# Optimization experiments

Measured on AMD Instinct MI355X. Metric: run time of the kernel, lower is better.

The kernel has to match this reference:

```python
import jax, jax.numpy as jnp
import numpy as np

NH = 16   # n_heads
HD = 64   # head_size
EMB = 1024  # n_embd = NH * HD
B, T = 4, 2048


def setup_inputs() -> dict:
    key = jax.random.key(0)
    k1, k2, k3 = jax.random.split(key, 3)
    x = jax.random.normal(k1, (B, T, EMB), dtype=jnp.float32)
    # torch Linear(in, out, bias=False): weight [out,in]; we store transposed [in,out]
    W_attn = jax.random.normal(k2, (EMB, 3 * NH * HD), dtype=jnp.float32) * (EMB ** -0.5)
    W_proj = jax.random.normal(k3, (NH * HD, EMB), dtype=jnp.float32) * ((NH * HD) ** -0.5)
    b_proj = jnp.zeros((EMB,), dtype=jnp.float32)
    return {"x": x, "W_attn": W_attn, "W_proj": W_proj, "b_proj": b_proj}


def reference(x, W_attn, W_proj, b_proj):
    Bq, Tq, C = x.shape
    qkv = x @ W_attn                      # [B,T,3*Nh*H]
    qs, ks, vs = jnp.split(qkv, 3, axis=2)
    def to_heads(t):                      # [B,T,Nh*H] -> [B,Nh,T,H]
        return t.reshape(Bq, Tq, NH, HD).transpose(0, 2, 1, 3)
    q, k, v = to_heads(qs), to_heads(ks), to_heads(vs)
    scores = jnp.einsum('bnth,bnsh->bnts', q, k) * (HD ** -0.5)  # [B,Nh,T,T]
    causal = jnp.tril(jnp.ones((Tq, Tq), dtype=bool))
    scores = jnp.where(causal, scores, -jnp.inf)
    attn = jax.nn.softmax(scores, axis=-1)
    # dropout is identity in eval mode
    y = jnp.einsum('bnts,bnsh->bnth', attn, v)                   # [B,Nh,T,H]
    y = y.transpose(0, 2, 1, 3).reshape(Bq, Tq, NH * HD)
    return y @ W_proj + b_proj
```

## Files before the change

kernel.cpp:

```cpp
#include <hip/hip_runtime.h>
#include <hip/hip_bf16.h>

#define NH 16
#define HD 64
#define EMB 1024
#define BB 4
#define TT 2048
#define MTOT (BB*TT)
#define N1 (3*NH*HD)
#define KD EMB

#define BM 128
#define BN 128
#define BK 32

#define QSCALE 0.18033688011112042f
#define FMAX 14.0f

typedef __bf16 bf16x8 __attribute__((ext_vector_type(8)));
typedef __bf16 bf16x4 __attribute__((ext_vector_type(4)));
typedef float  f32x4  __attribute__((ext_vector_type(4)));
typedef __hip_bfloat16 hbf;

__device__ __forceinline__ void async_copy16(const hbf* g, hbf* l) {
    __builtin_amdgcn_global_load_lds(
        (const __attribute__((address_space(1))) void*)g,
        (__attribute__((address_space(3))) void*)l, 16, 0, 0);
}

__device__ __forceinline__ bf16x4 pack4(float x0, float x1, float x2, float x3) {
    union { bf16x4 v; hbf a[4]; } u;
    u.a[0] = __float2bfloat16(x0);
    u.a[1] = __float2bfloat16(x1);
    u.a[2] = __float2bfloat16(x2);
    u.a[3] = __float2bfloat16(x3);
    return u.v;
}


__global__ __launch_bounds__(256) void f32_to_bf16_v4(const float* __restrict__ in,
                                                      hbf* __restrict__ out, int n4) {
    int i = blockIdx.x * blockDim.x + threadIdx.x;
    if (i < n4) {
        float4 v = ((const float4*)in)[i];
        *(bf16x4*)(out + 4 * (size_t)i) = pack4(v.x, v.y, v.z, v.w);
    }
}

__global__ __launch_bounds__(256) void f32_to_bf16_T(const float* __restrict__ in,
                                                     hbf* __restrict__ out, int R, int C) {
    __shared__ float T[64][65];
    int bc = blockIdx.x % (C / 64), br = blockIdx.x / (C / 64);
    int r0 = br * 64, c0 = bc * 64;
    int tr = threadIdx.x >> 6, tc = threadIdx.x & 63;
    #pragma unroll
    for (int i = 0; i < 16; ++i)
        T[4 * i + tr][tc] = in[(size_t)(r0 + 4 * i + tr) * C + c0 + tc];
    __syncthreads();
    #pragma unroll
    for (int i = 0; i < 16; ++i)
        out[(size_t)(c0 + 4 * i + tr) * R + r0 + tc] = __float2bfloat16(T[tc][4 * i + tr]);
}


#define GEMM_STAGE(Sdst, Gsrc, ld)                                            \
    {                                                                         \
        _Pragma("unroll")                                                     \
        for (int q = 0; q < 2; ++q) {                                         \
            int e = q * 2048 + tid * 8;                                       \
            int row = e >> 5, col = e & 31;                                   \
            async_copy16(Gsrc + (size_t)row * (ld) + col,                     \
                         Sdst + q * 2048 + (tid & ~63) * 8);                  \
        }                                                                     \
    }

__global__ __launch_bounds__(256) void gemm_qkv(
    const hbf* __restrict__ A, const hbf* __restrict__ Bt,
    hbf* __restrict__ qh, hbf* __restrict__ kh, hbf* __restrict__ vt)
{
    __shared__ __align__(16) hbf As[BM * BK];
    __shared__ __align__(16) hbf Bs[BN * BK];
    int tid = threadIdx.x;
    int wv = tid >> 6, lane = tid & 63;
    int g = lane >> 4, c = lane & 15;
    int wr = wv >> 1, wc = wv & 1;
    int bn = blockIdx.x % (N1 / BN);
    int bm = blockIdx.x / (N1 / BN);
    int m0 = bm * BM, n0 = bn * BN;

    f32x4 acc[4][4];
    #pragma unroll
    for (int i = 0; i < 4; ++i)
        #pragma unroll
        for (int j = 0; j < 4; ++j) acc[i][j] = (f32x4){0.f, 0.f, 0.f, 0.f};

    for (int k0 = 0; k0 < KD; k0 += BK) {
        const hbf* Ag = A  + (size_t)m0 * KD + k0;
        const hbf* Bg = Bt + (size_t)n0 * KD + k0;
        GEMM_STAGE(As, Ag, KD);
        GEMM_STAGE(Bs, Bg, KD);
        __syncthreads();
        bf16x8 af[4], bf[4];
        #pragma unroll
        for (int mi = 0; mi < 4; ++mi)
            af[mi] = *(const bf16x8*)(As + (wr * 64 + mi * 16 + c) * BK + g * 8);
        #pragma unroll
        for (int ni = 0; ni < 4; ++ni)
            bf[ni] = *(const bf16x8*)(Bs + (wc * 64 + ni * 16 + c) * BK + g * 8);
        #pragma unroll
        for (int mi = 0; mi < 4; ++mi)
            #pragma unroll
            for (int ni = 0; ni < 4; ++ni)
                acc[mi][ni] = __builtin_amdgcn_mfma_f32_16x16x32_bf16(af[mi], bf[ni], acc[mi][ni], 0, 0, 0);
        __syncthreads();
    }

    int colbase = n0 + wc * 64;
    int which = colbase / (NH * HD);
    int h = (colbase % (NH * HD)) / HD;
    int b = m0 / TT;
    float scale = (which == 0) ? QSCALE : 1.0f;
    if (which < 2) {
        hbf* dst = (which == 0) ? qh : kh;
        dst += ((size_t)b * NH + h) * TT * HD;
        #pragma unroll
        for (int mi = 0; mi < 4; ++mi)
            #pragma unroll
            for (int ni = 0; ni < 4; ++ni) {
                int d = ni * 16 + c;
                #pragma unroll
                for (int r = 0; r < 4; ++r) {
                    int t = (m0 + wr * 64 + mi * 16 + g * 4 + r) % TT;
                    dst[(size_t)t * HD + d] = __float2bfloat16(acc[mi][ni][r] * scale);
                }
            }
    } else {
        hbf* dst = vt + ((size_t)b * NH + h) * TT * HD;
        #pragma unroll
        for (int mi = 0; mi < 4; ++mi)
            #pragma unroll
            for (int ni = 0; ni < 4; ++ni) {
                int d = ni * 16 + c;
                #pragma unroll
                for (int r = 0; r < 4; ++r) {
                    int t = (m0 + wr * 64 + mi * 16 + g * 4 + r) % TT;
                    dst[(size_t)d * TT + t] = __float2bfloat16(acc[mi][ni][r]);
                }
            }
    }
}


__global__ __launch_bounds__(512, 4) void attn(
    const hbf* __restrict__ qh, const hbf* __restrict__ kh, const hbf* __restrict__ vt,
    hbf* __restrict__ y)
{
    __shared__ __align__(16) hbf Ks[128 * 64];
    __shared__ __align__(16) hbf Vs[64 * 128];
    __shared__ __align__(16) hbf Ps[8][16 * 64];

    int tid = threadIdx.x;
    int wv = tid >> 6, lane = tid & 63;
    int g = lane >> 4, c = lane & 15;
    int c7 = c & 7;

    int bh = blockIdx.x >> 3;
    int pi = blockIdx.x & 7;
    int b = bh >> 4, h = bh & 15;

    const hbf* Q = qh + (size_t)bh * TT * HD;
    const hbf* K = kh + (size_t)bh * TT * HD;
    const hbf* V = vt + (size_t)bh * TT * HD;
    hbf* Pq = &Ps[wv][0];

    union { bf16x8 v; hbf a[8]; } uo;
    #pragma unroll
    for (int i = 0; i < 8; ++i) uo.a[i] = __float2bfloat16(1.0f);
    const bf16x8 ones8 = uo.v;

    #pragma unroll
    for (int pass = 0; pass < 2; ++pass) {
        int sst = pass ? (15 - pi) : pi;
        int qb = sst * 128;
        int q0 = qb + wv * 16;
        int kend = q0 + 16;
        int kmax = qb + 128;

        bf16x8 aq0 = *(const bf16x8*)(Q + (size_t)(q0 + c) * HD + g * 8);
        bf16x8 aq1 = *(const bf16x8*)(Q + (size_t)(q0 + c) * HD + 32 + g * 8);

        f32x4 lacc = (f32x4){0.f, 0.f, 0.f, 0.f};
        f32x4 o[4];
        #pragma unroll
        for (int d = 0; d < 4; ++d) o[d] = (f32x4){0.f, 0.f, 0.f, 0.f};

        for (int k0 = 0; k0 < kmax; k0 += 128) {
            __syncthreads();
            #pragma unroll
            for (int it = 0; it < 2; ++it) {
                int e = it * 4096 + tid * 8;
                int key = e >> 6, sblk = (e >> 3) & 7;
                int dblk = sblk ^ (key & 7);
                async_copy16(K + (size_t)(k0 + key) * HD + dblk * 8,
                             Ks + it * 4096 + (tid & ~63) * 8);
            }
            #pragma unroll
            for (int it = 0; it < 2; ++it) {
                int e = it * 4096 + tid * 8;
                int dim = e >> 7, kb = (e >> 3) & 15;
                int skb = kb ^ (dim & 7);
                async_copy16(V + (size_t)dim * TT + k0 + skb * 8,
                             Vs + it * 4096 + (tid & ~63) * 8);
            }
            __syncthreads();

            #pragma unroll
            for (int ch = 0; ch < 2; ++ch) {
                int c64 = k0 + ch * 64;
                if (c64 < kend) {
                    f32x4 s[4];
                    #pragma unroll
                    for (int t = 0; t < 4; ++t) {
                        int kt = c64 + 16 * t;
                        if (kt < kend) {
                            int rb = (ch * 64 + 16 * t + c) * 64;
                            bf16x8 kf0 = *(const bf16x8*)(Ks + rb + ((g ^ c7) << 3));
                            bf16x8 kf1 = *(const bf16x8*)(Ks + rb + (((4 + g) ^ c7) << 3));
                            f32x4 a = (f32x4){-FMAX, -FMAX, -FMAX, -FMAX};
                            a = __builtin_amdgcn_mfma_f32_16x16x32_bf16(kf0, aq0, a, 0, 0, 0);
                            a = __builtin_amdgcn_mfma_f32_16x16x32_bf16(kf1, aq1, a, 0, 0, 0);
                            if (kt == q0) {
                                #pragma unroll
                                for (int r = 0; r < 4; ++r)
                                    a[r] = (g * 4 + r <= c) ? a[r] : -1e30f;
                            }
                            s[t] = a;
                        } else
                            s[t] = (f32x4){-1e30f, -1e30f, -1e30f, -1e30f};
                    }
                    #pragma unroll
                    for (int t = 0; t < 4; ++t) {
                        f32x4 e;
                        #pragma unroll
                        for (int r = 0; r < 4; ++r) e[r] = __builtin_amdgcn_exp2f(s[t][r]);
                        *(bf16x4*)(Pq + c * 64 + (((2 * t + (g >> 1)) ^ c7) << 3) + ((g & 1) << 2)) =
                            pack4(e[0], e[1], e[2], e[3]);
                    }
                    #pragma unroll
                    for (int sc = 0; sc < 2; ++sc) {
                        if (c64 + 32 * sc < kend) {
                            bf16x8 pf = *(const bf16x8*)(Pq + c * 64 + (((4 * sc + g) ^ c7) << 3));
                            lacc = __builtin_amdgcn_mfma_f32_16x16x32_bf16(ones8, pf, lacc, 0, 0, 0);
                            #pragma unroll
                            for (int d = 0; d < 4; ++d) {
                                int dim = d * 16 + c;
                                bf16x8 vf = *(const bf16x8*)(Vs + dim * 128 +
                                              (((ch * 8 + 4 * sc + g) ^ c7) << 3));
                                o[d] = __builtin_amdgcn_mfma_f32_16x16x32_bf16(vf, pf, o[d], 0, 0, 0);
                            }
                        }
                    }
                }
            }
        }

        float inv = 1.0f / lacc[0];
        #pragma unroll
        for (int d = 0; d < 4; ++d) {
            *(bf16x4*)(y + (size_t)(b * TT + q0 + c) * EMB + h * HD + d * 16 + g * 4) =
                pack4(o[d][0] * inv, o[d][1] * inv, o[d][2] * inv, o[d][3] * inv);
        }
    }
}


__global__ __launch_bounds__(256) void gemm_out(
    const hbf* __restrict__ A, const hbf* __restrict__ Bt,
    const float* __restrict__ bias, float* __restrict__ out)
{
    __shared__ __align__(16) hbf As[BM * BK];
    __shared__ __align__(16) hbf Bs[BN * BK];
    int tid = threadIdx.x;
    int wv = tid >> 6, lane = tid & 63;
    int g = lane >> 4, c = lane & 15;
    int wr = wv >> 1, wc = wv & 1;
    int bn = blockIdx.x % (EMB / BN);
    int bm = blockIdx.x / (EMB / BN);
    int m0 = bm * BM, n0 = bn * BN;

    f32x4 acc[4][4];
    #pragma unroll
    for (int i = 0; i < 4; ++i)
        #pragma unroll
        for (int j = 0; j < 4; ++j) acc[i][j] = (f32x4){0.f, 0.f, 0.f, 0.f};

    for (int k0 = 0; k0 < EMB; k0 += BK) {
        const hbf* Ag = A  + (size_t)m0 * EMB + k0;
        const hbf* Bg = Bt + (size_t)n0 * EMB + k0;
        GEMM_STAGE(As, Ag, EMB);
        GEMM_STAGE(Bs, Bg, EMB);
        __syncthreads();
        bf16x8 af[4], bf[4];
        #pragma unroll
        for (int mi = 0; mi < 4; ++mi)
            af[mi] = *(const bf16x8*)(As + (wr * 64 + mi * 16 + c) * BK + g * 8);
        #pragma unroll
        for (int ni = 0; ni < 4; ++ni)
            bf[ni] = *(const bf16x8*)(Bs + (wc * 64 + ni * 16 + c) * BK + g * 8);
        #pragma unroll
        for (int mi = 0; mi < 4; ++mi)
            #pragma unroll
            for (int ni = 0; ni < 4; ++ni)
                acc[mi][ni] = __builtin_amdgcn_mfma_f32_16x16x32_bf16(af[mi], bf[ni], acc[mi][ni], 0, 0, 0);
        __syncthreads();
    }

    #pragma unroll
    for (int mi = 0; mi < 4; ++mi)
        #pragma unroll
        for (int ni = 0; ni < 4; ++ni) {
            int col = n0 + wc * 64 + ni * 16 + c;
            float bv = bias[col];
            #pragma unroll
            for (int r = 0; r < 4; ++r) {
                int row = m0 + wr * 64 + mi * 16 + g * 4 + r;
                out[(size_t)row * EMB + col] = acc[mi][ni][r] + bv;
            }
        }
}


extern "C" void kernel_launch(void* const* d_in, const int* in_sizes, int n_in,
                              void* d_out, int out_size, void* d_ws, size_t ws_size,
                              hipStream_t stream)
{
    const float* x      = (const float*)d_in[0];
    const float* W_attn = (const float*)d_in[1];
    const float* W_proj = (const float*)d_in[2];
    const float* b_proj = (const float*)d_in[3];
    float* out = (float*)d_out;

    char* ws = (char*)d_ws;
    hbf* xb    = (hbf*)ws; ws += (size_t)MTOT * KD * 2;
    hbf* wab_t = (hbf*)ws; ws += (size_t)N1 * KD * 2;
    hbf* wpb_t = (hbf*)ws; ws += (size_t)EMB * EMB * 2;
    hbf* qh    = (hbf*)ws; ws += (size_t)MTOT * EMB * 2;
    hbf* kh    = (hbf*)ws; ws += (size_t)MTOT * EMB * 2;
    hbf* vt    = (hbf*)ws; ws += (size_t)MTOT * EMB * 2;
    hbf* yb    = (hbf*)ws; ws += (size_t)MTOT * EMB * 2;

    f32_to_bf16_v4<<<(MTOT * KD / 4 + 255) / 256, 256, 0, stream>>>(x, xb, MTOT * KD / 4);
    f32_to_bf16_T<<<(KD / 64) * (N1 / 64), 256, 0, stream>>>(W_attn, wab_t, KD, N1);
    f32_to_bf16_T<<<(KD / 64) * (EMB / 64), 256, 0, stream>>>(W_proj, wpb_t, KD, EMB);

    gemm_qkv<<<(MTOT / BM) * (N1 / BN), 256, 0, stream>>>(xb, wab_t, qh, kh, vt);
    attn<<<BB * NH * 8, 512, 0, stream>>>(qh, kh, vt, yb);
    gemm_out<<<(MTOT / BM) * (EMB / BN), 256, 0, stream>>>(yb, wpb_t, b_proj, out);
}
```

Measured before the change: 254.8 us.

## Replace both GEMMs with 8-wave double-buffered swizzled BK=64 kernel

```diff
diff --git a/kernel.cpp b/kernel.cpp
--- a/kernel.cpp
+++ b/kernel.cpp
@@ -10,10 +10,6 @@
 #define N1 (3*NH*HD)
 #define KD EMB
 
-#define BM 128
-#define BN 128
-#define BK 32
-
 #define QSCALE 0.18033688011112042f
 #define FMAX 14.0f
 
@@ -63,88 +59,143 @@
 }
 
 
-#define GEMM_STAGE(Sdst, Gsrc, ld)                                            \
-    {                                                                         \
-        _Pragma("unroll")                                                     \
-        for (int q = 0; q < 2; ++q) {                                         \
-            int e = q * 2048 + tid * 8;                                       \
-            int row = e >> 5, col = e & 31;                                   \
-            async_copy16(Gsrc + (size_t)row * (ld) + col,                     \
-                         Sdst + q * 2048 + (tid & ~63) * 8);                  \
-        }                                                                     \
-    }
-
-__global__ __launch_bounds__(256) void gemm_qkv(
+template<int NBN, int MODE>
+__global__ __launch_bounds__(512, 4) void gemm8(
     const hbf* __restrict__ A, const hbf* __restrict__ Bt,
-    hbf* __restrict__ qh, hbf* __restrict__ kh, hbf* __restrict__ vt)
+    hbf* __restrict__ qh, hbf* __restrict__ kh, hbf* __restrict__ vt,
+    const float* __restrict__ bias, float* __restrict__ out)
 {
-    __shared__ __align__(16) hbf As[BM * BK];
-    __shared__ __align__(16) hbf Bs[BN * BK];
+    constexpr int NKT = KD / 64;
+    __shared__ __align__(16) hbf As[2 * 128 * 64];
+    __shared__ __align__(16) hbf Bs[2 * 128 * 64];
+
     int tid = threadIdx.x;
     int wv = tid >> 6, lane = tid & 63;
     int g = lane >> 4, c = lane & 15;
-    int wr = wv >> 1, wc = wv & 1;
-    int bn = blockIdx.x % (N1 / BN);
-    int bm = blockIdx.x / (N1 / BN);
-    int m0 = bm * BM, n0 = bn * BN;
-
-    f32x4 acc[4][4];
+    int wm = wv >> 2, wn = wv & 3;
+    int bn = blockIdx.x % NBN, bm = blockIdx.x / NBN;
+    int m0 = bm * 128, n0 = bn * 128;
+
+    int sr0 = tid >> 3;
+    int sgc = (tid & 7) ^ (sr0 & 7);
+    const hbf* Asrc0 = A  + (size_t)(m0 + sr0) * KD + sgc * 8;
+    const hbf* Asrc1 = A  + (size_t)(m0 + 64 + sr0) * KD + sgc * 8;
+    const hbf* Bsrc0 = Bt + (size_t)(n0 + sr0) * KD + sgc * 8;
+    const hbf* Bsrc1 = Bt + (size_t)(n0 + 64 + sr0) * KD + sgc * 8;
+    int ldst0 = (tid & ~63) * 8;
+    int ldst1 = 4096 + (tid & ~63) * 8;
+
+#define STAGE_A8(tt, buf) { async_copy16(Asrc0 + (tt) * 64, As + (buf) * 8192 + ldst0); \
+                            async_copy16(Asrc1 + (tt) * 64, As + (buf) * 8192 + ldst1); }
+#define STAGE_B8(tt, buf) { async_copy16(Bsrc0 + (tt) * 64, Bs + (buf) * 8192 + ldst0); \
+                            async_copy16(Bsrc1 + (tt) * 64, Bs + (buf) * 8192 + ldst1); }
+
+    int xr = c & 7;
+    int aoff0 = (wm * 64 + c) * 64 + ((g ^ xr) << 3);
+    int aoff1 = (wm * 64 + c) * 64 + (((4 + g) ^ xr) << 3);
+    int boff0 = (wn * 32 + c) * 64 + ((g ^ xr) << 3);
+    int boff1 = (wn * 32 + c) * 64 + (((4 + g) ^ xr) << 3);
+
+    f32x4 acc[4][2];
     #pragma unroll
     for (int i = 0; i < 4; ++i)
         #pragma unroll
-        for (int j = 0; j < 4; ++j) acc[i][j] = (f32x4){0.f, 0.f, 0.f, 0.f};
-
-    for (int k0 = 0; k0 < KD; k0 += BK) {
-        const hbf* Ag = A  + (size_t)m0 * KD + k0;
-        const hbf* Bg = Bt + (size_t)n0 * KD + k0;
-        GEMM_STAGE(As, Ag, KD);
-        GEMM_STAGE(Bs, Bg, KD);
-        __syncthreads();
-        bf16x8 af[4], bf[4];
-        #pragma unroll
-        for (int mi = 0; mi < 4; ++mi)
-            af[mi] = *(const bf16x8*)(As + (wr * 64 + mi * 16 + c) * BK + g * 8);
-        #pragma unroll
-        for (int ni = 0; ni < 4; ++ni)
-            bf[ni] = *(const bf16x8*)(Bs + (wc * 64 + ni * 16 + c) * BK + g * 8);
-        #pragma unroll
-        for (int mi = 0; mi < 4; ++mi)
-            #pragma unroll
-            for (int ni = 0; ni < 4; ++ni)
-                acc[mi][ni] = __builtin_amdgcn_mfma_f32_16x16x32_bf16(af[mi], bf[ni], acc[mi][ni], 0, 0, 0);
-        __syncthreads();
+        for (int j = 0; j < 2; ++j) acc[i][j] = (f32x4){0.f, 0.f, 0.f, 0.f};
+
+    STAGE_A8(0, 0);
+    STAGE_B8(0, 0);
+    STAGE_A8(1, 1);
+    asm volatile("s_waitcnt vmcnt(2)" ::: "memory");
+    asm volatile("s_barrier" ::: "memory");
+    __builtin_amdgcn_sched_barrier(0);
+
+    for (int t = 0; t < NKT; ++t) {
+        int cur = t & 1;
+        const hbf* Ab = As + cur * 8192;
+        const hbf* Bb = Bs + cur * 8192;
+        bf16x8 af[4][2], bfr[2];
+        #pragma unroll
+        for (int i = 0; i < 4; ++i) {
+            af[i][0] = *(const bf16x8*)(Ab + aoff0 + i * 1024);
+            af[i][1] = *(const bf16x8*)(Ab + aoff1 + i * 1024);
+        }
+        bfr[0] = *(const bf16x8*)(Bb + boff0);
+        bfr[1] = *(const bf16x8*)(Bb + boff1);
+        if (t + 1 < NKT) STAGE_B8(t + 1, cur ^ 1);
+        __builtin_amdgcn_s_setprio(1);
+        #pragma unroll
+        for (int i = 0; i < 4; ++i) {
+            acc[i][0] = __builtin_amdgcn_mfma_f32_16x16x32_bf16(af[i][0], bfr[0], acc[i][0], 0, 0, 0);
+            acc[i][0] = __builtin_amdgcn_mfma_f32_16x16x32_bf16(af[i][1], bfr[1], acc[i][0], 0, 0, 0);
+        }
+        __builtin_amdgcn_s_setprio(0);
+        asm volatile("s_barrier" ::: "memory");
+        __builtin_amdgcn_sched_barrier(0);
+        bfr[0] = *(const bf16x8*)(Bb + boff0 + 1024);
+        bfr[1] = *(const bf16x8*)(Bb + boff1 + 1024);
+        if (t + 2 < NKT) STAGE_A8(t + 2, cur);
+        __builtin_amdgcn_s_setprio(1);
+        #pragma unroll
+        for (int i = 0; i < 4; ++i) {
+            acc[i][1] = __builtin_amdgcn_mfma_f32_16x16x32_bf16(af[i][0], bfr[0], acc[i][1], 0, 0, 0);
+            acc[i][1] = __builtin_amdgcn_mfma_f32_16x16x32_bf16(af[i][1], bfr[1], acc[i][1], 0, 0, 0);
+        }
+        __builtin_amdgcn_s_setprio(0);
+        if (t + 2 < NKT) { asm volatile("s_waitcnt vmcnt(2)" ::: "memory"); }
+        else             { asm volatile("s_waitcnt vmcnt(0)" ::: "memory"); }
+        asm volatile("s_barrier" ::: "memory");
+        __builtin_amdgcn_sched_barrier(0);
     }
 
-    int colbase = n0 + wc * 64;
-    int which = colbase / (NH * HD);
-    int h = (colbase % (NH * HD)) / HD;
-    int b = m0 / TT;
-    float scale = (which == 0) ? QSCALE : 1.0f;
-    if (which < 2) {
-        hbf* dst = (which == 0) ? qh : kh;
-        dst += ((size_t)b * NH + h) * TT * HD;
-        #pragma unroll
-        for (int mi = 0; mi < 4; ++mi)
-            #pragma unroll
-            for (int ni = 0; ni < 4; ++ni) {
-                int d = ni * 16 + c;
+#undef STAGE_A8
+#undef STAGE_B8
+
+    if constexpr (MODE == 0) {
+        int colbase = n0 + wn * 32;
+        int which = colbase >> 10;
+        int h = (colbase & 1023) >> 6;
+        int dbase = colbase & 63;
+        int b = m0 / TT;
+        int trow = (m0 % TT) + wm * 64;
+        if (which < 2) {
+            float scale = (which == 0) ? QSCALE : 1.0f;
+            hbf* dst = ((which == 0) ? qh : kh) + ((size_t)b * NH + h) * TT * HD;
+            #pragma unroll
+            for (int i = 0; i < 4; ++i)
+                #pragma unroll
+                for (int nf = 0; nf < 2; ++nf) {
+                    int d = dbase + nf * 16 + c;
+                    #pragma unroll
+                    for (int r = 0; r < 4; ++r) {
+                        int trw = trow + i * 16 + g * 4 + r;
+                        dst[(size_t)trw * HD + d] = __float2bfloat16(acc[i][nf][r] * scale);
+                    }
+                }
+        } else {
+            hbf* dst = vt + ((size_t)b * NH + h) * TT * HD;
+            #pragma unroll
+            for (int i = 0; i < 4; ++i)
+                #pragma unroll
+                for (int nf = 0; nf < 2; ++nf) {
+                    int d = dbase + nf * 16 + c;
+                    #pragma unroll
+                    for (int r = 0; r < 4; ++r) {
+                        int trw = trow + i * 16 + g * 4 + r;
+                        dst[(size_t)d * TT + trw] = __float2bfloat16(acc[i][nf][r]);
+                    }
+                }
+        }
+    } else {
+        #pragma unroll
+        for (int i = 0; i < 4; ++i)
+            #pragma unroll
+            for (int nf = 0; nf < 2; ++nf) {
+                int col = n0 + wn * 32 + nf * 16 + c;
+                float bv = bias[col];
                 #pragma unroll
                 for (int r = 0; r < 4; ++r) {
-                    int t = (m0 + wr * 64 + mi * 16 + g * 4 + r) % TT;
-                    dst[(size_t)t * HD + d] = __float2bfloat16(acc[mi][ni][r] * scale);
-                }
-            }
-    } else {
-        hbf* dst = vt + ((size_t)b * NH + h) * TT * HD;
-        #pragma unroll
-        for (int mi = 0; mi < 4; ++mi)
-            #pragma unroll
-            for (int ni = 0; ni < 4; ++ni) {
-                int d = ni * 16 + c;
-                #pragma unroll
-                for (int r = 0; r < 4; ++r) {
-                    int t = (m0 + wr * 64 + mi * 16 + g * 4 + r) % TT;
-                    dst[(size_t)d * TT + t] = __float2bfloat16(acc[mi][ni][r]);
+                    int row = m0 + wm * 64 + i * 16 + g * 4 + r;
+                    out[(size_t)row * EMB + col] = acc[i][nf][r] + bv;
                 }
             }
     }
@@ -274,62 +325,6 @@
 }
 
 
-__global__ __launch_bounds__(256) void gemm_out(
-    const hbf* __restrict__ A, const hbf* __restrict__ Bt,
-    const float* __restrict__ bias, float* __restrict__ out)
-{
-    __shared__ __align__(16) hbf As[BM * BK];
-    __shared__ __align__(16) hbf Bs[BN * BK];
-    int tid = threadIdx.x;
-    int wv = tid >> 6, lane = tid & 63;
-    int g = lane >> 4, c = lane & 15;
-    int wr = wv >> 1, wc = wv & 1;
-    int bn = blockIdx.x % (EMB / BN);
-    int bm = blockIdx.x / (EMB / BN);
-    int m0 = bm * BM, n0 = bn * BN;
-
-    f32x4 acc[4][4];
-    #pragma unroll
-    for (int i = 0; i < 4; ++i)
-        #pragma unroll
-        for (int j = 0; j < 4; ++j) acc[i][j] = (f32x4){0.f, 0.f, 0.f, 0.f};
-
-    for (int k0 = 0; k0 < EMB; k0 += BK) {
-        const hbf* Ag = A  + (size_t)m0 * EMB + k0;
-        const hbf* Bg = Bt + (size_t)n0 * EMB + k0;
-        GEMM_STAGE(As, Ag, EMB);
-        GEMM_STAGE(Bs, Bg, EMB);
-        __syncthreads();
-        bf16x8 af[4], bf[4];
-        #pragma unroll
-        for (int mi = 0; mi < 4; ++mi)
-            af[mi] = *(const bf16x8*)(As + (wr * 64 + mi * 16 + c) * BK + g * 8);
-        #pragma unroll
-        for (int ni = 0; ni < 4; ++ni)
-            bf[ni] = *(const bf16x8*)(Bs + (wc * 64 + ni * 16 + c) * BK + g * 8);
-        #pragma unroll
-        for (int mi = 0; mi < 4; ++mi)
-            #pragma unroll
-            for (int ni = 0; ni < 4; ++ni)
-                acc[mi][ni] = __builtin_amdgcn_mfma_f32_16x16x32_bf16(af[mi], bf[ni], acc[mi][ni], 0, 0, 0);
-        __syncthreads();
-    }
-
-    #pragma unroll
-    for (int mi = 0; mi < 4; ++mi)
-        #pragma unroll
-        for (int ni = 0; ni < 4; ++ni) {
-            int col = n0 + wc * 64 + ni * 16 + c;
-            float bv = bias[col];
-            #pragma unroll
-            for (int r = 0; r < 4; ++r) {
-                int row = m0 + wr * 64 + mi * 16 + g * 4 + r;
-                out[(size_t)row * EMB + col] = acc[mi][ni][r] + bv;
-            }
-        }
-}
-
-
 extern "C" void kernel_launch(void* const* d_in, const int* in_sizes, int n_in,
                               void* d_out, int out_size, void* d_ws, size_t ws_size,
                               hipStream_t stream)
@@ -353,7 +348,9 @@
     f32_to_bf16_T<<<(KD / 64) * (N1 / 64), 256, 0, stream>>>(W_attn, wab_t, KD, N1);
     f32_to_bf16_T<<<(KD / 64) * (EMB / 64), 256, 0, stream>>>(W_proj, wpb_t, KD, EMB);
 
-    gemm_qkv<<<(MTOT / BM) * (N1 / BN), 256, 0, stream>>>(xb, wab_t, qh, kh, vt);
+    gemm8<N1 / 128, 0><<<(MTOT / 128) * (N1 / 128), 512, 0, stream>>>(
+        xb, wab_t, qh, kh, vt, nullptr, nullptr);
     attn<<<BB * NH * 8, 512, 0, stream>>>(qh, kh, vt, yb);
-    gemm_out<<<(MTOT / BM) * (EMB / BN), 256, 0, stream>>>(yb, wpb_t, b_proj, out);
-}
+    gemm8<EMB / 128, 1><<<(MTOT / 128) * (EMB / 128), 512, 0, stream>>>(
+        yb, wpb_t, nullptr, nullptr, nullptr, b_proj, out);
+}
```

New measurement: 254.2 us. About the same (-0.3%).
